# Kernel optimization log

Hardware: AMD Instinct MI355X
Metric: run time of the kernel (lower is better)

## Reference

```python
import jax, jax.numpy as jnp
import numpy as np

N_NODES = 50000
N_EDGES = 800000
NODE_INV_DIM = 64   # h_channels(32) * num_l0(2)
H_DIM = 128         # edge_channels_list[0]
IN_DIM = H_DIM + 2 * NODE_INV_DIM  # 256
LN_EPS = 1e-5


def setup_inputs() -> dict:
    key = jax.random.key(0)
    ks = jax.random.split(key, 10)
    node_inv = jax.random.normal(ks[0], (N_NODES, NODE_INV_DIM), dtype=jnp.float32)
    edge_features = jax.random.normal(ks[1], (N_EDGES, H_DIM), dtype=jnp.float32)
    edge_src = jax.random.randint(ks[2], (N_EDGES,), 0, N_NODES, dtype=jnp.int32).astype(jnp.int64)
    edge_dst = jax.random.randint(ks[3], (N_EDGES,), 0, N_NODES, dtype=jnp.int32).astype(jnp.int64)
    # MLP + LayerNorm params (PyTorch default-ish init scale)
    W1 = jax.random.normal(ks[4], (IN_DIM, H_DIM), dtype=jnp.float32) / np.sqrt(IN_DIM)
    b1 = jnp.zeros((H_DIM,), dtype=jnp.float32)
    W2 = jax.random.normal(ks[5], (H_DIM, H_DIM), dtype=jnp.float32) / np.sqrt(H_DIM)
    b2 = jnp.zeros((H_DIM,), dtype=jnp.float32)
    gamma = jnp.ones((H_DIM,), dtype=jnp.float32)
    beta = jnp.zeros((H_DIM,), dtype=jnp.float32)
    return {"node_inv": node_inv, "edge_features": edge_features,
            "edge_src": edge_src, "edge_dst": edge_dst,
            "W1": W1, "b1": b1, "W2": W2, "b2": b2,
            "gamma": gamma, "beta": beta}


def _layer_norm(x, gamma, beta):
    mu = jnp.mean(x, axis=-1, keepdims=True)
    var = jnp.mean((x - mu) ** 2, axis=-1, keepdims=True)
    return (x - mu) * jax.lax.rsqrt(var + LN_EPS) * gamma + beta


def reference(node_inv, edge_features, edge_src, edge_dst, W1, b1, W2, b2, gamma, beta):
    # Irregular gather: node invariant features for each edge endpoint. [E, 64]
    src_feat = jnp.take(node_inv, edge_src, axis=0)
    dst_feat = jnp.take(node_inv, edge_dst, axis=0)
    # Concat -> [E, 256]
    in_features = jnp.concatenate([src_feat, dst_feat, edge_features], axis=-1)
    # 2-layer MLP with ReLU
    h = jax.nn.relu(in_features @ W1 + b1)
    update = h @ W2 + b2
    # Residual add of LayerNorm(update)
    return edge_features + _layer_norm(update, gamma, beta)
```

## Files before the change

kernel.cpp:

```cpp
#include <hip/hip_runtime.h>
#include <stdint.h>

typedef _Float16 half8 __attribute__((ext_vector_type(8)));
typedef float f32x4 __attribute__((ext_vector_type(4)));

constexpr int E_EDGES = 800000;
constexpr int HD = 128;
constexpr int RS = 136;

__global__ __launch_bounds__(256) void pack_weights(
    const float* __restrict__ W1, const float* __restrict__ W2,
    _Float16* __restrict__ W1p, _Float16* __restrict__ W2p)
{
    int t = blockIdx.x * 256 + threadIdx.x;
    if (t < 32768) {
        int j = t & 7, lane = (t >> 3) & 63, nt = (t >> 9) & 7, ks = t >> 12;
        int k = ks * 32 + (lane >> 4) * 8 + j;
        int n = nt * 16 + (lane & 15);
        W1p[t] = (_Float16)W1[k * HD + n];
    } else if (t < 49152) {
        int q = t - 32768;
        int j = q & 7, lane = (q >> 3) & 63, nt = (q >> 9) & 7, ks = q >> 12;
        int k = ks * 32 + (lane >> 4) * 8 + j;
        int n = nt * 16 + (lane & 15);
        W2p[q] = (_Float16)W2[k * HD + n];
    }
}

__global__ __launch_bounds__(256, 2) void edge_update(
    const float* __restrict__ node_inv,
    const float* __restrict__ edge_feat,
    const int* __restrict__ esrc,
    const int* __restrict__ edst,
    const float* __restrict__ b1v,
    const float* __restrict__ b2v,
    const float* __restrict__ gammav,
    const float* __restrict__ betav,
    const _Float16* __restrict__ W1p,
    const _Float16* __restrict__ W2p,
    float* __restrict__ out)
{
    __shared__ __align__(16) _Float16 hl[4 * 32 * RS];

    const int tid  = threadIdx.x;
    const int lane = tid & 63;
    const int w    = tid >> 6;
    const int quad = lane >> 4;
    const int c    = lane & 15;
    const int rb   = blockIdx.x * 128 + w * 32;
    const int rA0  = rb + c;
    const int rA1  = rb + 16 + c;

    const int s0 = esrc[rA0], d0 = edst[rA0];
    const int s1 = esrc[rA1], d1 = edst[rA1];

    f32x4 acc[2][8];
#pragma unroll
    for (int nt = 0; nt < 8; ++nt) {
        float bv = b1v[nt * 16 + c];
        acc[0][nt] = (f32x4){bv, bv, bv, bv};
        acc[1][nt] = acc[0][nt];
    }

#pragma unroll
    for (int ks = 0; ks < 8; ++ks) {
        const int k0 = ks * 32 + quad * 8;
        const float *pa0, *pa1;
        if (ks < 2) {
            pa0 = node_inv + (long long)s0 * 64 + k0;
            pa1 = node_inv + (long long)s1 * 64 + k0;
        } else if (ks < 4) {
            pa0 = node_inv + (long long)d0 * 64 + (k0 - 64);
            pa1 = node_inv + (long long)d1 * 64 + (k0 - 64);
        } else {
            pa0 = edge_feat + (long long)rA0 * HD + (k0 - 128);
            pa1 = edge_feat + (long long)rA1 * HD + (k0 - 128);
        }
        float4 x00 = ((const float4*)pa0)[0];
        float4 x01 = ((const float4*)pa0)[1];
        float4 x10 = ((const float4*)pa1)[0];
        float4 x11 = ((const float4*)pa1)[1];
        half8 a0, a1;
        a0[0]=(_Float16)x00.x; a0[1]=(_Float16)x00.y; a0[2]=(_Float16)x00.z; a0[3]=(_Float16)x00.w;
        a0[4]=(_Float16)x01.x; a0[5]=(_Float16)x01.y; a0[6]=(_Float16)x01.z; a0[7]=(_Float16)x01.w;
        a1[0]=(_Float16)x10.x; a1[1]=(_Float16)x10.y; a1[2]=(_Float16)x10.z; a1[3]=(_Float16)x10.w;
        a1[4]=(_Float16)x11.x; a1[5]=(_Float16)x11.y; a1[6]=(_Float16)x11.z; a1[7]=(_Float16)x11.w;
#pragma unroll
        for (int nt = 0; nt < 8; ++nt) {
            half8 b = *(const half8*)(W1p + (((ks * 8 + nt) * 64 + lane) << 3));
            acc[0][nt] = __builtin_amdgcn_mfma_f32_16x16x32_f16(a0, b, acc[0][nt], 0, 0, 0);
            acc[1][nt] = __builtin_amdgcn_mfma_f32_16x16x32_f16(a1, b, acc[1][nt], 0, 0, 0);
        }
    }

    _Float16* hw = hl + w * 32 * RS;
#pragma unroll
    for (int m = 0; m < 2; ++m)
#pragma unroll
        for (int nt = 0; nt < 8; ++nt)
#pragma unroll
            for (int r = 0; r < 4; ++r) {
                float v = acc[m][nt][r];
                v = v > 0.f ? v : 0.f;
                hw[(m * 16 + quad * 4 + r) * RS + nt * 16 + c] = (_Float16)v;
            }
    __syncthreads();

#pragma unroll
    for (int nt = 0; nt < 8; ++nt) {
        float bv = b2v[nt * 16 + c];
        acc[0][nt] = (f32x4){bv, bv, bv, bv};
        acc[1][nt] = acc[0][nt];
    }
#pragma unroll
    for (int ks = 0; ks < 4; ++ks) {
        half8 a0 = *(const half8*)(hw + c * RS + ks * 32 + quad * 8);
        half8 a1 = *(const half8*)(hw + (16 + c) * RS + ks * 32 + quad * 8);
#pragma unroll
        for (int nt = 0; nt < 8; ++nt) {
            half8 b = *(const half8*)(W2p + (((ks * 8 + nt) * 64 + lane) << 3));
            acc[0][nt] = __builtin_amdgcn_mfma_f32_16x16x32_f16(a0, b, acc[0][nt], 0, 0, 0);
            acc[1][nt] = __builtin_amdgcn_mfma_f32_16x16x32_f16(a1, b, acc[1][nt], 0, 0, 0);
        }
    }

    float gv[8], btv[8];
#pragma unroll
    for (int nt = 0; nt < 8; ++nt) {
        gv[nt]  = gammav[nt * 16 + c];
        btv[nt] = betav[nt * 16 + c];
    }

#pragma unroll
    for (int m = 0; m < 2; ++m) {
        float sum[4] = {0, 0, 0, 0}, sq[4] = {0, 0, 0, 0};
#pragma unroll
        for (int nt = 0; nt < 8; ++nt)
#pragma unroll
            for (int r = 0; r < 4; ++r) {
                float v = acc[m][nt][r];
                sum[r] += v;
                sq[r]  += v * v;
            }
#pragma unroll
        for (int mask = 1; mask < 16; mask <<= 1)
#pragma unroll
            for (int r = 0; r < 4; ++r) {
                sum[r] += __shfl_xor(sum[r], mask);
                sq[r]  += __shfl_xor(sq[r], mask);
            }
        float mu[4], rstd[4];
#pragma unroll
        for (int r = 0; r < 4; ++r) {
            mu[r] = sum[r] * (1.0f / 128.0f);
            float var = sq[r] * (1.0f / 128.0f) - mu[r] * mu[r];
            rstd[r] = rsqrtf(var + 1e-5f);
        }
        const int rowg = rb + m * 16 + quad * 4;
#pragma unroll
        for (int nt = 0; nt < 8; ++nt)
#pragma unroll
            for (int r = 0; r < 4; ++r) {
                long long idx = (long long)(rowg + r) * HD + nt * 16 + c;
                out[idx] = edge_feat[idx] + (acc[m][nt][r] - mu[r]) * rstd[r] * gv[nt] + btv[nt];
            }
    }
}

extern "C" void kernel_launch(void* const* d_in, const int* in_sizes, int n_in,
                              void* d_out, int out_size, void* d_ws, size_t ws_size,
                              hipStream_t stream)
{
    const float* node_inv  = (const float*)d_in[0];
    const float* edge_feat = (const float*)d_in[1];
    const int*   esrc      = (const int*)d_in[2];
    const int*   edst      = (const int*)d_in[3];
    const float* W1        = (const float*)d_in[4];
    const float* b1        = (const float*)d_in[5];
    const float* W2        = (const float*)d_in[6];
    const float* b2        = (const float*)d_in[7];
    const float* gamma     = (const float*)d_in[8];
    const float* beta      = (const float*)d_in[9];

    _Float16* W1p = (_Float16*)d_ws;
    _Float16* W2p = W1p + 32768;

    pack_weights<<<192, 256, 0, stream>>>(W1, W2, W1p, W2p);
    edge_update<<<E_EDGES / 128, 256, 0, stream>>>(node_inv, edge_feat, esrc, edst,
                                                   b1, b2, gamma, beta, W1p, W2p,
                                                   (float*)d_out);
}
```

Baseline: 974.4 us.

## Prefetch all A operands up front, split GEMM1 by N halves, raise occupancy

All gathered node and edge features for both row tiles are loaded and converted to fp16 before any MFMA, so the loads go out together instead of one k-step at a time. GEMM1 is split into two N-halves of 4 tiles each, which shrinks the live accumulator set, and launch bounds ask for 4 blocks per SM instead of 2. The residual edge_feat values are loaded before the LayerNorm reductions, and the output uses nontemporal stores. The aim is more memory-level parallelism and more resident waves to hide gather latency, with a risk of register spills under the tighter bound.

```diff
diff --git a/kernel.cpp b/kernel.cpp
--- a/kernel.cpp
+++ b/kernel.cpp
@@ -27,7 +27,15 @@
     }
 }
 
-__global__ __launch_bounds__(256, 2) void edge_update(
+__device__ __forceinline__ half8 cvt8(float4 a, float4 b)
+{
+    half8 h;
+    h[0] = (_Float16)a.x; h[1] = (_Float16)a.y; h[2] = (_Float16)a.z; h[3] = (_Float16)a.w;
+    h[4] = (_Float16)b.x; h[5] = (_Float16)b.y; h[6] = (_Float16)b.z; h[7] = (_Float16)b.w;
+    return h;
+}
+
+__global__ __launch_bounds__(256, 4) void edge_update(
     const float* __restrict__ node_inv,
     const float* __restrict__ edge_feat,
     const int* __restrict__ esrc,
@@ -54,62 +62,92 @@
     const int s0 = esrc[rA0], d0 = edst[rA0];
     const int s1 = esrc[rA1], d1 = edst[rA1];
 
+    const float* ps0 = node_inv + (long long)s0 * 64 + quad * 8;
+    const float* pd0 = node_inv + (long long)d0 * 64 + quad * 8;
+    const float* pe0 = edge_feat + (long long)rA0 * HD + quad * 8;
+    const float* ps1 = node_inv + (long long)s1 * 64 + quad * 8;
+    const float* pd1 = node_inv + (long long)d1 * 64 + quad * 8;
+    const float* pe1 = edge_feat + (long long)rA1 * HD + quad * 8;
+
+    half8 xa0[8], xa1[8];
+    {
+        float4 xf[16];
+#pragma unroll
+        for (int ks = 0; ks < 8; ++ks) {
+            const float* pa = ks < 2 ? ps0 + ks * 32
+                            : ks < 4 ? pd0 + (ks - 2) * 32
+                                     : pe0 + (ks - 4) * 32;
+            xf[ks * 2]     = ((const float4*)pa)[0];
+            xf[ks * 2 + 1] = ((const float4*)pa)[1];
+        }
+#pragma unroll
+        for (int ks = 0; ks < 8; ++ks)
+            xa0[ks] = cvt8(xf[ks * 2], xf[ks * 2 + 1]);
+    }
+    {
+        float4 xf[16];
+#pragma unroll
+        for (int ks = 0; ks < 8; ++ks) {
+            const float* pa = ks < 2 ? ps1 + ks * 32
+                            : ks < 4 ? pd1 + (ks - 2) * 32
+                                     : pe1 + (ks - 4) * 32;
+            xf[ks * 2]     = ((const float4*)pa)[0];
+            xf[ks * 2 + 1] = ((const float4*)pa)[1];
+        }
+#pragma unroll
+        for (int ks = 0; ks < 8; ++ks)
+            xa1[ks] = cvt8(xf[ks * 2], xf[ks * 2 + 1]);
+    }
+
+    float bini[8];
+#pragma unroll
+    for (int nt = 0; nt < 8; ++nt) bini[nt] = b1v[nt * 16 + c];
+
+    _Float16* hw = hl + w * 32 * RS;
+
+#pragma unroll
+    for (int nh = 0; nh < 2; ++nh) {
+        f32x4 a0c[4], a1c[4];
+#pragma unroll
+        for (int nt = 0; nt < 4; ++nt) {
+            float bv = bini[nh * 4 + nt];
+            a0c[nt] = (f32x4){bv, bv, bv, bv};
+            a1c[nt] = a0c[nt];
+        }
+#pragma unroll
+        for (int ks = 0; ks < 8; ++ks) {
+#pragma unroll
+            for (int nt = 0; nt < 4; ++nt) {
+                half8 bfr = *(const half8*)(W1p + (((ks * 8 + nh * 4 + nt) * 64 + lane) << 3));
+                a0c[nt] = __builtin_amdgcn_mfma_f32_16x16x32_f16(xa0[ks], bfr, a0c[nt], 0, 0, 0);
+                a1c[nt] = __builtin_amdgcn_mfma_f32_16x16x32_f16(xa1[ks], bfr, a1c[nt], 0, 0, 0);
+            }
+        }
+#pragma unroll
+        for (int nt = 0; nt < 4; ++nt)
+#pragma unroll
+            for (int r = 0; r < 4; ++r) {
+                float v0 = a0c[nt][r]; v0 = v0 > 0.f ? v0 : 0.f;
+                hw[(quad * 4 + r) * RS + nh * 64 + nt * 16 + c] = (_Float16)v0;
+                float v1 = a1c[nt][r]; v1 = v1 > 0.f ? v1 : 0.f;
+                hw[(16 + quad * 4 + r) * RS + nh * 64 + nt * 16 + c] = (_Float16)v1;
+            }
+    }
+
+    __syncthreads();
+
+    float b2i[8], gv[8], btv[8];
+#pragma unroll
+    for (int nt = 0; nt < 8; ++nt) {
+        b2i[nt] = b2v[nt * 16 + c];
+        gv[nt]  = gammav[nt * 16 + c];
+        btv[nt] = betav[nt * 16 + c];
+    }
+
     f32x4 acc[2][8];
 #pragma unroll
     for (int nt = 0; nt < 8; ++nt) {
-        float bv = b1v[nt * 16 + c];
-        acc[0][nt] = (f32x4){bv, bv, bv, bv};
-        acc[1][nt] = acc[0][nt];
-    }
-
-#pragma unroll
-    for (int ks = 0; ks < 8; ++ks) {
-        const int k0 = ks * 32 + quad * 8;
-        const float *pa0, *pa1;
-        if (ks < 2) {
-            pa0 = node_inv + (long long)s0 * 64 + k0;
-            pa1 = node_inv + (long long)s1 * 64 + k0;
-        } else if (ks < 4) {
-            pa0 = node_inv + (long long)d0 * 64 + (k0 - 64);
-            pa1 = node_inv + (long long)d1 * 64 + (k0 - 64);
-        } else {
-            pa0 = edge_feat + (long long)rA0 * HD + (k0 - 128);
-            pa1 = edge_feat + (long long)rA1 * HD + (k0 - 128);
-        }
-        float4 x00 = ((const float4*)pa0)[0];
-        float4 x01 = ((const float4*)pa0)[1];
-        float4 x10 = ((const float4*)pa1)[0];
-        float4 x11 = ((const float4*)pa1)[1];
-        half8 a0, a1;
-        a0[0]=(_Float16)x00.x; a0[1]=(_Float16)x00.y; a0[2]=(_Float16)x00.z; a0[3]=(_Float16)x00.w;
-        a0[4]=(_Float16)x01.x; a0[5]=(_Float16)x01.y; a0[6]=(_Float16)x01.z; a0[7]=(_Float16)x01.w;
-        a1[0]=(_Float16)x10.x; a1[1]=(_Float16)x10.y; a1[2]=(_Float16)x10.z; a1[3]=(_Float16)x10.w;
-        a1[4]=(_Float16)x11.x; a1[5]=(_Float16)x11.y; a1[6]=(_Float16)x11.z; a1[7]=(_Float16)x11.w;
-#pragma unroll
-        for (int nt = 0; nt < 8; ++nt) {
-            half8 b = *(const half8*)(W1p + (((ks * 8 + nt) * 64 + lane) << 3));
-            acc[0][nt] = __builtin_amdgcn_mfma_f32_16x16x32_f16(a0, b, acc[0][nt], 0, 0, 0);
-            acc[1][nt] = __builtin_amdgcn_mfma_f32_16x16x32_f16(a1, b, acc[1][nt], 0, 0, 0);
-        }
-    }
-
-    _Float16* hw = hl + w * 32 * RS;
-#pragma unroll
-    for (int m = 0; m < 2; ++m)
-#pragma unroll
-        for (int nt = 0; nt < 8; ++nt)
-#pragma unroll
-            for (int r = 0; r < 4; ++r) {
-                float v = acc[m][nt][r];
-                v = v > 0.f ? v : 0.f;
-                hw[(m * 16 + quad * 4 + r) * RS + nt * 16 + c] = (_Float16)v;
-            }
-    __syncthreads();
-
-#pragma unroll
-    for (int nt = 0; nt < 8; ++nt) {
-        float bv = b2v[nt * 16 + c];
-        acc[0][nt] = (f32x4){bv, bv, bv, bv};
+        acc[0][nt] = (f32x4){b2i[nt], b2i[nt], b2i[nt], b2i[nt]};
         acc[1][nt] = acc[0][nt];
     }
 #pragma unroll
@@ -118,21 +156,23 @@
         half8 a1 = *(const half8*)(hw + (16 + c) * RS + ks * 32 + quad * 8);
 #pragma unroll
         for (int nt = 0; nt < 8; ++nt) {
-            half8 b = *(const half8*)(W2p + (((ks * 8 + nt) * 64 + lane) << 3));
-            acc[0][nt] = __builtin_amdgcn_mfma_f32_16x16x32_f16(a0, b, acc[0][nt], 0, 0, 0);
-            acc[1][nt] = __builtin_amdgcn_mfma_f32_16x16x32_f16(a1, b, acc[1][nt], 0, 0, 0);
-        }
-    }
-
-    float gv[8], btv[8];
-#pragma unroll
-    for (int nt = 0; nt < 8; ++nt) {
-        gv[nt]  = gammav[nt * 16 + c];
-        btv[nt] = betav[nt * 16 + c];
+            half8 bfr = *(const half8*)(W2p + (((ks * 8 + nt) * 64 + lane) << 3));
+            acc[0][nt] = __builtin_amdgcn_mfma_f32_16x16x32_f16(a0, bfr, acc[0][nt], 0, 0, 0);
+            acc[1][nt] = __builtin_amdgcn_mfma_f32_16x16x32_f16(a1, bfr, acc[1][nt], 0, 0, 0);
+        }
     }
 
 #pragma unroll
     for (int m = 0; m < 2; ++m) {
+        const int rowg = rb + m * 16 + quad * 4;
+
+        float res[8][4];
+#pragma unroll
+        for (int nt = 0; nt < 8; ++nt)
+#pragma unroll
+            for (int r = 0; r < 4; ++r)
+                res[nt][r] = edge_feat[(long long)(rowg + r) * HD + nt * 16 + c];
+
         float sum[4] = {0, 0, 0, 0}, sq[4] = {0, 0, 0, 0};
 #pragma unroll
         for (int nt = 0; nt < 8; ++nt)
@@ -156,13 +196,13 @@
             float var = sq[r] * (1.0f / 128.0f) - mu[r] * mu[r];
             rstd[r] = rsqrtf(var + 1e-5f);
         }
-        const int rowg = rb + m * 16 + quad * 4;
 #pragma unroll
         for (int nt = 0; nt < 8; ++nt)
 #pragma unroll
             for (int r = 0; r < 4; ++r) {
                 long long idx = (long long)(rowg + r) * HD + nt * 16 + c;
-                out[idx] = edge_feat[idx] + (acc[m][nt][r] - mu[r]) * rstd[r] * gv[nt] + btv[nt];
+                float v = res[nt][r] + (acc[m][nt][r] - mu[r]) * rstd[r] * gv[nt] + btv[nt];
+                __builtin_nontemporal_store(v, &out[idx]);
             }
     }
 }
```

Result: faster. 892.3 us (-8.4%).
